# Optimization experiments

Hardware: AMD Instinct MI355X
Metric: run time of the kernel (lower is better)

The kernel has to match this reference:

```python
import jax, jax.numpy as jnp
import numpy as np

C, D, B, NS = 1000, 256, 16384, 200000
MOMENTUM = 0.1
TOPK = 5
EPS = 1e-12  # torch F.normalize default eps


def _cos_distance(a, b):
    # 0.5 * (1 - cos_sim) between rows of a [N,D] and rows of b [M,D]
    a = a / jnp.maximum(jnp.linalg.norm(a, axis=1, keepdims=True), EPS)
    b = b / jnp.maximum(jnp.linalg.norm(b, axis=1, keepdims=True), EPS)
    return 0.5 * (1.0 - jnp.einsum('nd,md->nm', a, b))


def setup_inputs() -> dict:
    key = jax.random.key(0)
    k1, k2, k3, k4 = jax.random.split(key, 4)
    return {
        'feature_source': jax.random.normal(k1, (B, D), jnp.float32),
        'center_mem': jax.random.normal(k2, (C, D), jnp.float32),
        'source_mem': jax.random.normal(k3, (NS, D), jnp.float32),
        'class2center': jnp.zeros((C, 2), jnp.float32),
        'interdist': jnp.zeros((C, C, 2), jnp.float32),
        'label_source': jax.random.randint(k4, (B,), 0, C, jnp.int32),
        'index_source': jnp.arange(B, dtype=jnp.int32),
    }


def reference(feature_source, center_mem, source_mem, class2center, interdist,
              label_source, index_source):
    # --- featuredistance2center: scatter-add per-class count and distance ---
    d1 = _cos_distance(feature_source, center_mem)            # [B, C]
    dist_at_label = jnp.take_along_axis(d1, label_source[:, None], axis=1)[:, 0]  # [B]
    class2center_new = class2center.at[label_source, 0].add(1.0)
    class2center_new = class2center_new.at[label_source, 1].add(dist_at_label)

    # --- update_center (labels_value=None): center += sum of features per class ---
    center_new = center_mem + jax.ops.segment_sum(feature_source, label_source,
                                                  num_segments=C)  # [C, D]

    # --- update_source: momentum scatter update of the source feature bank ---
    old = source_mem[index_source]                             # [B, D]
    source_mem_new = source_mem.at[index_source].set((1.0 - MOMENTUM) * old
                                                     + MOMENTUM * feature_source)

    # --- sourcefeature2differertcenter: topk-smallest distances, scatter-add ---
    d2 = _cos_distance(feature_source, center_new)             # [B, C]
    neg_vals, top_idx = jax.lax.top_k(-d2, TOPK)               # smallest distances
    top_dists = -neg_vals                                      # [B, TOPK]
    top1, top2 = top_idx[:, 0], top_idx[:, 1]
    inter = jnp.abs(top_dists[:, 0] - top_dists[:, 1])         # [B]
    interdist_new = interdist.at[top1, top2, 0].add(1.0)
    interdist_new = interdist_new.at[top1, top2, 1].add(inter)

    return (center_new, source_mem_new, class2center_new, interdist_new)
```

## Files before the change

kernel.cpp:

```cpp
#include <hip/hip_runtime.h>
#include <math.h>

#define Cc 1000
#define Cpad 1024
#define Dd 256
#define Bb 16384
#define NSs 200000
#define MOM 0.1f
#define EPSV 1e-12f
#define EPSC 0.10f
#define NEG_BIG (-3.4e38f)
#define IDX_BIG 0x7fffffff

#define OUT_CENTER 0
#define OUT_SRC (Cc*Dd)
#define OUT_C2C (OUT_SRC + (size_t)NSs*Dd)
#define OUT_INTER (OUT_C2C + Cc*2)

#define SCR_SCORES 0
#define SCR_FB 8388608
#define SCR_CB (SCR_FB + 2097152)
#define SCR_END 10616832
#define SAFE_ROW 41472
#define E0 (SAFE_ROW * 64)
#define N4ALL (NSs * 64)

#define WS_CHAT 0
#define WS_INVF 256000
#define WS_MARK 272384

typedef __bf16    bf16x8 __attribute__((ext_vector_type(8)));
typedef float     f32x4  __attribute__((ext_vector_type(4)));
typedef _Float16  f16x8  __attribute__((ext_vector_type(8)));

__device__ __forceinline__ ushort f2bf(float f) {
    uint u = __float_as_uint(f);
    u += 0x7FFFu + ((u >> 16) & 1u);
    return (ushort)(u >> 16);
}

__device__ __forceinline__ void gload16(const void* g, void* l) {
    __builtin_amdgcn_global_load_lds(
        (const __attribute__((address_space(1))) void*)g,
        (__attribute__((address_space(3))) void*)l, 16, 0, 0);
}

__device__ __forceinline__ void upd_top2(float& s1, int& i1, float& s2, int& i2,
                                         float s, int i) {
    if (s > s1 || (s == s1 && i < i1)) {
        s2 = s1; i2 = i1; s1 = s; i1 = i;
    } else if (s > s2 || (s == s2 && i < i2)) {
        s2 = s; i2 = i;
    }
}

__device__ __forceinline__ void copy_range(const float* __restrict__ src,
                                           const float* __restrict__ feat,
                                           const int* __restrict__ mark,
                                           float* __restrict__ dst,
                                           int e0, int e1, int tid0, int nthreads) {
    for (int e = e0 + tid0; e < e1; e += nthreads) {
        int row = e >> 6;
        int m = mark[row];
        f32x4 v = __builtin_nontemporal_load((const f32x4*)src + e);
        if (m >= 0) {
            f32x4 f = *((const f32x4*)feat + (size_t)m * 64 + (e & 63));
            v = (1.0f - MOM) * v + MOM * f;
        }
        __builtin_nontemporal_store(v, (f32x4*)dst + e);
    }
}

#define N_INTER4 (Cc*Cc*2/4)
#define N_C2C4   (Cc*2/4)
#define N_CM4    (Cc*Dd/4)
#define N_MARK4  (NSs/4)
#define N_INIT4  (N_INTER4 + N_C2C4 + N_CM4 + N_MARK4)

__global__ void k_init(const float4* __restrict__ interdist,
                       const float4* __restrict__ c2c,
                       const float4* __restrict__ cmem,
                       float4* __restrict__ out_inter,
                       float4* __restrict__ out_c2c,
                       float4* __restrict__ out_center,
                       int4* __restrict__ mark) {
    int i = blockIdx.x * blockDim.x + threadIdx.x;
    if (i < N_INTER4) {
        out_inter[i] = interdist[i];
    } else if (i < N_INTER4 + N_C2C4) {
        out_c2c[i - N_INTER4] = c2c[i - N_INTER4];
    } else if (i < N_INTER4 + N_C2C4 + N_CM4) {
        out_center[i - N_INTER4 - N_C2C4] = cmem[i - N_INTER4 - N_C2C4];
    } else if (i < N_INIT4) {
        int4 m; m.x = -1; m.y = -1; m.z = -1; m.w = -1;
        mark[i - N_INTER4 - N_C2C4 - N_CM4] = m;
    }
}

__global__ void k_rows_a(const float* __restrict__ feat, const float* __restrict__ cmem,
                         const int* __restrict__ label, const int* __restrict__ index,
                         float* __restrict__ out_center, float* __restrict__ out_c2c,
                         float* __restrict__ ws_invf, ushort* __restrict__ fb,
                         int* __restrict__ mark) {
    int wid  = threadIdx.x >> 6;
    int lane = threadIdx.x & 63;
    int row  = blockIdx.x * 4 + wid;
    if (row >= Bb) return;

    const float4 f4 = *(const float4*)(feat + (size_t)row * Dd + lane * 4);
    int lab = label[row];
    const float4 c4 = *(const float4*)(cmem + (size_t)lab * Dd + lane * 4);

    ushort4 h;
    h.x = f2bf(f4.x); h.y = f2bf(f4.y); h.z = f2bf(f4.z); h.w = f2bf(f4.w);
    *(ushort4*)(fb + (size_t)row * Dd + lane * 4) = h;

    float fs = f4.x*f4.x + f4.y*f4.y + f4.z*f4.z + f4.w*f4.w;
    float dt = f4.x*c4.x + f4.y*c4.y + f4.z*c4.z + f4.w*c4.w;
    float cs = c4.x*c4.x + c4.y*c4.y + c4.z*c4.z + c4.w*c4.w;
    #pragma unroll
    for (int off = 32; off; off >>= 1) {
        fs += __shfl_xor(fs, off);
        dt += __shfl_xor(dt, off);
        cs += __shfl_xor(cs, off);
    }
    float invf = 1.0f / fmaxf(sqrtf(fs), EPSV);
    if (lane == 0) {
        ws_invf[row] = invf;
        mark[index[row]] = row;
        float invc = 1.0f / fmaxf(sqrtf(cs), EPSV);
        float d1 = 0.5f * (1.0f - dt * invf * invc);
        atomicAdd(out_c2c + lab * 2,     1.0f);
        atomicAdd(out_c2c + lab * 2 + 1, d1);
    }
    atomicAdd(out_center + (size_t)lab * Dd + lane * 4 + 0, f4.x);
    atomicAdd(out_center + (size_t)lab * Dd + lane * 4 + 1, f4.y);
    atomicAdd(out_center + (size_t)lab * Dd + lane * 4 + 2, f4.z);
    atomicAdd(out_center + (size_t)lab * Dd + lane * 4 + 3, f4.w);
}

__global__ void k_chat(const float* __restrict__ out_center, float* __restrict__ chat,
                       ushort* __restrict__ cb) {
    int c = blockIdx.x;
    int lane = threadIdx.x;
    if (c >= Cc) {
        ushort4 z; z.x = 0; z.y = 0; z.z = 0; z.w = 0;
        *(ushort4*)(cb + (size_t)c * Dd + lane * 4) = z;
        return;
    }
    float4 v = *(const float4*)(out_center + (size_t)c * Dd + lane * 4);
    float ss = v.x*v.x + v.y*v.y + v.z*v.z + v.w*v.w;
    #pragma unroll
    for (int off = 32; off; off >>= 1) ss += __shfl_xor(ss, off);
    float inv = 1.0f / fmaxf(sqrtf(ss), EPSV);
    float4 r; r.x = v.x*inv; r.y = v.y*inv; r.z = v.z*inv; r.w = v.w*inv;
    *(float4*)(chat + (size_t)c * Dd + lane * 4) = r;
    ushort4 h;
    h.x = f2bf(r.x); h.y = f2bf(r.y); h.z = f2bf(r.z); h.w = f2bf(r.w);
    *(ushort4*)(cb + (size_t)c * Dd + lane * 4) = h;
}

#define GEMM_BLKS 1024
#define COPY_BLKS 3072
#define TOTAL_BLKS 4096

__global__ __launch_bounds__(256, 3) void k_gemm_copy(const ushort* __restrict__ fb,
                                                      const ushort* __restrict__ cb,
                                                      _Float16* __restrict__ scores,
                                                      const float* __restrict__ smem,
                                                      const float* __restrict__ feat,
                                                      const int* __restrict__ mark,
                                                      float* __restrict__ out_src) {
    __shared__ __align__(16) char Asb[128 * 128];
    __shared__ __align__(16) char Bsb[128 * 128];

    int b = blockIdx.x;
    if ((b & 3) != 0) {
        int c = (b - (b >> 2)) - 1;
        int tid0 = c * 256 + threadIdx.x;
        copy_range(smem, feat, mark, out_src, E0, N4ALL, tid0, COPY_BLKS * 256);
        return;
    }
    int g = b >> 2;
    int bx = g & 7;
    int by = g >> 3;

    int tid  = threadIdx.x;
    int wid  = tid >> 6;
    int lane = tid & 63;
    int rl = lane & 15;
    int kg = lane >> 4;
    int wr = wid >> 1;
    int wc = wid & 1;
    int row0 = by * 128;
    int c0   = bx * 128;

    int realb = ((lane & 7) ^ (lane >> 3)) << 4;

    f32x4 acc[4][4];
    f32x4 z = {0.f, 0.f, 0.f, 0.f};
    #pragma unroll
    for (int mi = 0; mi < 4; mi++)
        #pragma unroll
        for (int ni = 0; ni < 4; ni++)
            acc[mi][ni] = z;

    for (int t = 0; t < 4; t++) {
        #pragma unroll
        for (int i = 0; i < 4; i++) {
            int rloc = wid * 32 + i * 8;
            int grow = row0 + rloc + (lane >> 3);
            gload16((const char*)(fb + (size_t)grow * Dd) + t * 128 + realb,
                    Asb + rloc * 128);
        }
        #pragma unroll
        for (int i = 0; i < 4; i++) {
            int rloc = wid * 32 + i * 8;
            int gcol = c0 + rloc + (lane >> 3);
            gload16((const char*)(cb + (size_t)gcol * Dd) + t * 128 + realb,
                    Bsb + rloc * 128);
        }
        asm volatile("s_waitcnt vmcnt(0)" ::: "memory");
        __syncthreads();

        bf16x8 a[4][2], bfr[4][2];
        #pragma unroll
        for (int mi = 0; mi < 4; mi++)
            #pragma unroll
            for (int ks = 0; ks < 2; ks++) {
                int r = wr * 64 + mi * 16 + rl;
                int off = r * 128 + ((ks * 64 + kg * 16) ^ ((r & 7) << 4));
                a[mi][ks] = *(const bf16x8*)(Asb + off);
            }
        #pragma unroll
        for (int ni = 0; ni < 4; ni++)
            #pragma unroll
            for (int ks = 0; ks < 2; ks++) {
                int r = wc * 64 + ni * 16 + rl;
                int off = r * 128 + ((ks * 64 + kg * 16) ^ ((r & 7) << 4));
                bfr[ni][ks] = *(const bf16x8*)(Bsb + off);
            }

        #pragma unroll
        for (int ks = 0; ks < 2; ks++)
            #pragma unroll
            for (int mi = 0; mi < 4; mi++)
                #pragma unroll
                for (int ni = 0; ni < 4; ni++)
                    acc[mi][ni] = __builtin_amdgcn_mfma_f32_16x16x32_bf16(
                        a[mi][ks], bfr[ni][ks], acc[mi][ni], 0, 0, 0);

        __syncthreads();
    }

    #pragma unroll
    for (int mi = 0; mi < 4; mi++) {
        int row = row0 + wr * 64 + mi * 16 + kg * 4;
        #pragma unroll
        for (int ni = 0; ni < 4; ni++) {
            int col = c0 + wc * 64 + ni * 16 + rl;
            #pragma unroll
            for (int rr = 0; rr < 4; rr++)
                scores[(size_t)(row + rr) * Cpad + col] = (_Float16)acc[mi][ni][rr];
        }
    }
}

__global__ __launch_bounds__(256) void k_sel(const _Float16* __restrict__ scores,
                                             const float* __restrict__ feat,
                                             const float* __restrict__ chat,
                                             const float* __restrict__ ws_invf,
                                             float* __restrict__ out_inter) {
    __shared__ int cnt[4];
    __shared__ int clist[4][32];
    int wid  = threadIdx.x >> 6;
    int lane = threadIdx.x & 63;
    int row  = blockIdx.x * 4 + wid;
    if (lane == 0) cnt[wid] = 0;

    const f16x8* sp = (const f16x8*)(scores + (size_t)row * Cpad);
    float v[16];
    float s1 = NEG_BIG, s2 = NEG_BIG;
    int   i1 = IDX_BIG, i2 = IDX_BIG;
    #pragma unroll
    for (int k = 0; k < 2; k++) {
        f16x8 q = sp[k * 64 + lane];
        int cbase = k * 512 + lane * 8;
        #pragma unroll
        for (int e = 0; e < 8; e++) {
            float f = (float)q[e];
            v[k*8 + e] = f;
            int c = cbase + e;
            if (c < Cc) upd_top2(s1, i1, s2, i2, f, c);
        }
    }
    #pragma unroll
    for (int off = 1; off < 64; off <<= 1) {
        float ps1 = __shfl_xor(s1, off), ps2 = __shfl_xor(s2, off);
        int   pi1 = __shfl_xor(i1, off), pi2 = __shfl_xor(i2, off);
        upd_top2(s1, i1, s2, i2, ps1, pi1);
        upd_top2(s1, i1, s2, i2, ps2, pi2);
    }
    float thr = s2 - EPSC;
    #pragma unroll
    for (int j = 0; j < 16; j++) {
        int c = (j >> 3) * 512 + lane * 8 + (j & 7);
        if (v[j] >= thr && c < Cc) {
            int slot = atomicAdd(&cnt[wid], 1);
            if (slot < 32) clist[wid][slot] = c;
        }
    }
    __syncthreads();
    int n = cnt[wid]; if (n > 32) n = 32;

    const float4 f4 = *(const float4*)(feat + (size_t)row * Dd + lane * 4);
    float S1 = NEG_BIG, S2 = NEG_BIG;
    int   I1 = IDX_BIG, I2 = IDX_BIG;
    for (int k = 0; k < n; k++) {
        int c = clist[wid][k];
        const float4 c4 = *(const float4*)(chat + (size_t)c * Dd + lane * 4);
        float d = f4.x*c4.x + f4.y*c4.y + f4.z*c4.z + f4.w*c4.w;
        #pragma unroll
        for (int off = 32; off; off >>= 1) d += __shfl_xor(d, off);
        upd_top2(S1, I1, S2, I2, d, c);
    }
    if (lane == 0) {
        float inter = 0.5f * ws_invf[row] * (S1 - S2);
        size_t off2 = ((size_t)I1 * Cc + I2) * 2;
        atomicAdd(out_inter + off2,     1.0f);
        atomicAdd(out_inter + off2 + 1, inter);
    }
}

__global__ void k_src2(const float* __restrict__ src, const float* __restrict__ feat,
                       const int* __restrict__ mark, float* __restrict__ dst) {
    int tid0 = blockIdx.x * blockDim.x + threadIdx.x;
    copy_range(src, feat, mark, dst, 0, E0, tid0, gridDim.x * blockDim.x);
}

extern "C" void kernel_launch(void* const* d_in, const int* in_sizes, int n_in,
                              void* d_out, int out_size, void* d_ws, size_t ws_size,
                              hipStream_t stream) {
    const float* feat   = (const float*)d_in[0];
    const float* cmem   = (const float*)d_in[1];
    const float* smem   = (const float*)d_in[2];
    const float* c2c    = (const float*)d_in[3];
    const float* inter  = (const float*)d_in[4];
    const int*   label  = (const int*)d_in[5];
    const int*   index  = (const int*)d_in[6];

    float* out = (float*)d_out;
    float* out_center = out + OUT_CENTER;
    float* out_src    = out + OUT_SRC;
    float* out_c2c    = out + OUT_C2C;
    float* out_inter  = out + OUT_INTER;

    float* ws    = (float*)d_ws;
    float* chat  = ws + WS_CHAT;
    float* winvf = ws + WS_INVF;
    int*   mark  = (int*)(ws + WS_MARK);

    _Float16* scores = (_Float16*)(out_src + SCR_SCORES);
    ushort*   fb     = (ushort*)(out_src + SCR_FB);
    ushort*   cb     = (ushort*)(out_src + SCR_CB);

    k_init<<<(N_INIT4 + 255) / 256, 256, 0, stream>>>(
        (const float4*)inter, (const float4*)c2c, (const float4*)cmem,
        (float4*)out_inter, (float4*)out_c2c, (float4*)out_center,
        (int4*)mark);
    k_rows_a<<<Bb / 4, 256, 0, stream>>>(feat, cmem, label, index,
                                         out_center, out_c2c, winvf, fb, mark);
    k_chat<<<Cpad, 64, 0, stream>>>(out_center, chat, cb);
    k_gemm_copy<<<TOTAL_BLKS, 256, 0, stream>>>(fb, cb, scores,
                                                smem, feat, mark, out_src);
    k_sel<<<Bb / 4, 256, 0, stream>>>(scores, feat, chat, winvf, out_inter);
    k_src2<<<2048, 256, 0, stream>>>(smem, feat, mark, out_src);
}
```

Baseline: 253.1 us.

## Fold tail source-bank copy into selection kernel and use workspace scratch when large

Removes the separate k_src2 launch. When the workspace is too small, the rows of the output source bank that hold scratch data are copied inside k_sel, after each block has finished with its own scores rows. When the workspace is large enough, scores and the bf16 operands go into the workspace instead, so the whole bank copy runs in the GEMM kernel alongside the matmul. This saves a launch and lets the copy overlap compute. The price is a more complex ownership scheme that relies on each k_sel block reading only the scores region it later overwrites.

```diff
diff --git a/kernel.cpp b/kernel.cpp
--- a/kernel.cpp
+++ b/kernel.cpp
@@ -20,14 +20,18 @@
 #define SCR_SCORES 0
 #define SCR_FB 8388608
 #define SCR_CB (SCR_FB + 2097152)
-#define SCR_END 10616832
 #define SAFE_ROW 41472
 #define E0 (SAFE_ROW * 64)
+#define E_OWN_END 2097152
 #define N4ALL (NSs * 64)
 
 #define WS_CHAT 0
 #define WS_INVF 256000
 #define WS_MARK 272384
+#define WS_SCORES 472384
+#define WS_FB  (WS_SCORES + 8388608)
+#define WS_CB  (WS_FB + 2097152)
+#define WS_NEED_FLOATS 11089216
 
 typedef __bf16    bf16x8 __attribute__((ext_vector_type(8)));
 typedef float     f32x4  __attribute__((ext_vector_type(4)));
@@ -54,21 +58,18 @@
     }
 }
 
-__device__ __forceinline__ void copy_range(const float* __restrict__ src,
-                                           const float* __restrict__ feat,
-                                           const int* __restrict__ mark,
-                                           float* __restrict__ dst,
-                                           int e0, int e1, int tid0, int nthreads) {
-    for (int e = e0 + tid0; e < e1; e += nthreads) {
-        int row = e >> 6;
-        int m = mark[row];
-        f32x4 v = __builtin_nontemporal_load((const f32x4*)src + e);
-        if (m >= 0) {
-            f32x4 f = *((const f32x4*)feat + (size_t)m * 64 + (e & 63));
-            v = (1.0f - MOM) * v + MOM * f;
-        }
-        __builtin_nontemporal_store(v, (f32x4*)dst + e);
-    }
+__device__ __forceinline__ void copy_elem(const float* __restrict__ src,
+                                          const float* __restrict__ feat,
+                                          const int* __restrict__ mark,
+                                          float* __restrict__ dst, int e) {
+    int row = e >> 6;
+    int m = mark[row];
+    f32x4 v = __builtin_nontemporal_load((const f32x4*)src + e);
+    if (m >= 0) {
+        f32x4 f = *((const f32x4*)feat + (size_t)m * 64 + (e & 63));
+        v = (1.0f - MOM) * v + MOM * f;
+    }
+    __builtin_nontemporal_store(v, (f32x4*)dst + e);
 }
 
 #define N_INTER4 (Cc*Cc*2/4)
@@ -160,7 +161,6 @@
     *(ushort4*)(cb + (size_t)c * Dd + lane * 4) = h;
 }
 
-#define GEMM_BLKS 1024
 #define COPY_BLKS 3072
 #define TOTAL_BLKS 4096
 
@@ -170,7 +170,8 @@
                                                       const float* __restrict__ smem,
                                                       const float* __restrict__ feat,
                                                       const int* __restrict__ mark,
-                                                      float* __restrict__ out_src) {
+                                                      float* __restrict__ out_src,
+                                                      int e0copy) {
     __shared__ __align__(16) char Asb[128 * 128];
     __shared__ __align__(16) char Bsb[128 * 128];
 
@@ -178,7 +179,8 @@
     if ((b & 3) != 0) {
         int c = (b - (b >> 2)) - 1;
         int tid0 = c * 256 + threadIdx.x;
-        copy_range(smem, feat, mark, out_src, E0, N4ALL, tid0, COPY_BLKS * 256);
+        for (int e = e0copy + tid0; e < N4ALL; e += COPY_BLKS * 256)
+            copy_elem(smem, feat, mark, out_src, e);
         return;
     }
     int g = b >> 2;
@@ -270,7 +272,11 @@
                                              const float* __restrict__ feat,
                                              const float* __restrict__ chat,
                                              const float* __restrict__ ws_invf,
-                                             float* __restrict__ out_inter) {
+                                             float* __restrict__ out_inter,
+                                             const float* __restrict__ smem,
+                                             const int* __restrict__ mark,
+                                             float* __restrict__ out_src,
+                                             int doCopy) {
     __shared__ int cnt[4];
     __shared__ int clist[4][32];
     int wid  = threadIdx.x >> 6;
@@ -330,12 +336,18 @@
         atomicAdd(out_inter + off2,     1.0f);
         atomicAdd(out_inter + off2 + 1, inter);
     }
-}
-
-__global__ void k_src2(const float* __restrict__ src, const float* __restrict__ feat,
-                       const int* __restrict__ mark, float* __restrict__ dst) {
-    int tid0 = blockIdx.x * blockDim.x + threadIdx.x;
-    copy_range(src, feat, mark, dst, 0, E0, tid0, gridDim.x * blockDim.x);
+
+    if (doCopy) {
+        int base = blockIdx.x * 512;
+        #pragma unroll
+        for (int it = 0; it < 2; it++) {
+            int e = base + it * 256 + threadIdx.x;
+            copy_elem(smem, feat, mark, out_src, e);
+        }
+        for (int e = E_OWN_END + blockIdx.x * 256 + threadIdx.x; e < E0;
+             e += (Bb / 4) * 256)
+            copy_elem(smem, feat, mark, out_src, e);
+    }
 }
 
 extern "C" void kernel_launch(void* const* d_in, const int* in_sizes, int n_in,
@@ -360,9 +372,23 @@
     float* winvf = ws + WS_INVF;
     int*   mark  = (int*)(ws + WS_MARK);
 
-    _Float16* scores = (_Float16*)(out_src + SCR_SCORES);
-    ushort*   fb     = (ushort*)(out_src + SCR_FB);
-    ushort*   cb     = (ushort*)(out_src + SCR_CB);
+    bool wsbig = ws_size >= (size_t)WS_NEED_FLOATS * 4;
+    _Float16* scores;
+    ushort *fb, *cb;
+    int e0copy, doCopy;
+    if (wsbig) {
+        scores = (_Float16*)(ws + WS_SCORES);
+        fb     = (ushort*)(ws + WS_FB);
+        cb     = (ushort*)(ws + WS_CB);
+        e0copy = 0;
+        doCopy = 0;
+    } else {
+        scores = (_Float16*)(out_src + SCR_SCORES);
+        fb     = (ushort*)(out_src + SCR_FB);
+        cb     = (ushort*)(out_src + SCR_CB);
+        e0copy = E0;
+        doCopy = 1;
+    }
 
     k_init<<<(N_INIT4 + 255) / 256, 256, 0, stream>>>(
         (const float4*)inter, (const float4*)c2c, (const float4*)cmem,
@@ -372,7 +398,7 @@
                                          out_center, out_c2c, winvf, fb, mark);
     k_chat<<<Cpad, 64, 0, stream>>>(out_center, chat, cb);
     k_gemm_copy<<<TOTAL_BLKS, 256, 0, stream>>>(fb, cb, scores,
-                                                smem, feat, mark, out_src);
-    k_sel<<<Bb / 4, 256, 0, stream>>>(scores, feat, chat, winvf, out_inter);
-    k_src2<<<2048, 256, 0, stream>>>(smem, feat, mark, out_src);
-}
+                                                smem, feat, mark, out_src, e0copy);
+    k_sel<<<Bb / 4, 256, 0, stream>>>(scores, feat, chat, winvf, out_inter,
+                                      smem, mark, out_src, doCopy);
+}
```

Result: slower. 258.7 us (+2.2%).
